# Kernel optimization log

Hardware: AMD Instinct MI355X
Metric: run time of the kernel (lower is better)

## Reference

```python
import jax, jax.numpy as jnp
import numpy as np

B, F, D, K = 16384, 200, 32, 4
H1, H2 = 32, 16
BN_EPS = 1e-3  # keras BatchNormalization default epsilon


def setup_inputs() -> dict:
    key = jax.random.key(0)
    ks = jax.random.split(key, 12)
    inp = {
        "x": jax.random.normal(ks[0], (B, F, D), dtype=jnp.float32),
        "tag_embedding": jax.random.normal(ks[1], (B, D), dtype=jnp.float32),
        "vk_embs": jax.random.normal(ks[2], (D, K), dtype=jnp.float32) * 0.1,
        # tower 1: Dense(D->H1) stacked over K experts, + BN params
        "W1": jax.random.normal(ks[3], (K, D, H1), dtype=jnp.float32) * (1.0 / np.sqrt(D)),
        "b1": jnp.zeros((K, H1), dtype=jnp.float32),
        "g1": jnp.ones((K, H1), dtype=jnp.float32) + 0.1 * jax.random.normal(ks[4], (K, H1), dtype=jnp.float32),
        "be1": 0.1 * jax.random.normal(ks[5], (K, H1), dtype=jnp.float32),
        "m1": 0.1 * jax.random.normal(ks[6], (K, H1), dtype=jnp.float32),
        "v1": jax.random.uniform(ks[7], (K, H1), dtype=jnp.float32, minval=0.5, maxval=1.5),
        # tower 2: Dense(H1->H2) + BN params
        "W2": jax.random.normal(ks[8], (K, H1, H2), dtype=jnp.float32) * (1.0 / np.sqrt(H1)),
        "b2": jnp.zeros((K, H2), dtype=jnp.float32),
        "g2": jnp.ones((K, H2), dtype=jnp.float32) + 0.1 * jax.random.normal(ks[9], (K, H2), dtype=jnp.float32),
        "be2": 0.1 * jax.random.normal(ks[10], (K, H2), dtype=jnp.float32),
        "m2": 0.1 * jax.random.normal(ks[11], (K, H2), dtype=jnp.float32),
        "v2": jnp.ones((K, H2), dtype=jnp.float32),
    }
    return inp


def _bn(h, gamma, beta, mean, var):
    # inference-mode batch norm per expert, broadcast over batch: h [B,K,H]
    return (h - mean) * jax.lax.rsqrt(var + BN_EPS) * gamma + beta


def reference(x, tag_embedding, vk_embs, W1, b1, g1, be1, m1, v1,
              W2, b2, g2, be2, m2, v2):
    scale = 1.0 / jnp.sqrt(jnp.float32(D))
    # attention-pooled per-kernel context (dropout = identity in eval mode)
    vk_scores = jnp.einsum('bfd,dk->bkf', x, vk_embs)          # [B,K,F]
    vk_probs = jax.nn.softmax(vk_scores, axis=-1)
    context = jnp.einsum('bkf,bfd->bkd', vk_probs, x) * scale   # [B,K,D]
    # per-expert MLP towers, batched over K: Dense -> BN -> relu (dropout=id)
    h = jnp.einsum('bkd,kdh->bkh', context, W1) + b1            # [B,K,H1]
    h = jax.nn.relu(_bn(h, g1, be1, m1, v1))
    h = jnp.einsum('bkh,khj->bkj', h, W2) + b2                  # [B,K,H2]
    vk_outs = jax.nn.relu(_bn(h, g2, be2, m2, v2))
    # soft gate from tag embedding
    gate_scores = (tag_embedding @ vk_embs) * scale             # [B,K]
    gate_probs = jax.nn.softmax(gate_scores, axis=-1)[:, :, None]
    user_embedding = jnp.sum(vk_outs * gate_probs, axis=1)      # [B,H2]
    return user_embedding
```

## Files before the change

### kernel.cpp

```cpp
#include <hip/hip_runtime.h>
#include <hip/hip_bf16.h>

#define NF 200
#define ND 32
#define NK 4
#define NH1 32
#define NH2 16
#define BN_EPS 1e-3f

__global__ __launch_bounds__(256) void mvke_fused(
    const float* __restrict__ x, const float* __restrict__ tag,
    const float* __restrict__ vk,
    const float* __restrict__ W1, const float* __restrict__ b1,
    const float* __restrict__ g1, const float* __restrict__ be1,
    const float* __restrict__ m1, const float* __restrict__ v1,
    const float* __restrict__ W2, const float* __restrict__ b2,
    const float* __restrict__ g2, const float* __restrict__ be2,
    const float* __restrict__ m2, const float* __restrict__ v2,
    float* __restrict__ out, int nrows)
{
  __shared__ float w1s[NK*ND*NH1];
  __shared__ float w2s[NK*NH1*NH2];
  __shared__ float a1s[NK*NH1], c1s[NK*NH1];
  __shared__ float a2s[NK*NH2], c2s[NK*NH2];
  __shared__ float ctx_s[4][NK*ND];
  __shared__ float h1_s[4][NK*NH1];

  const int tid = threadIdx.x;
  for (int i = tid; i < NK*ND*NH1; i += 256) w1s[i] = W1[i];
  for (int i = tid; i < NK*NH1*NH2; i += 256) w2s[i] = W2[i];
  if (tid < NK*NH1) {
    const float a = g1[tid] * rsqrtf(v1[tid] + BN_EPS);
    a1s[tid] = a;
    c1s[tid] = (b1[tid] - m1[tid]) * a + be1[tid];
  } else if (tid >= 128 && tid < 128 + NK*NH2) {
    const int t = tid - 128;
    const float a = g2[t] * rsqrtf(v2[t] + BN_EPS);
    a2s[t] = a;
    c2s[t] = (b2[t] - m2[t]) * a + be2[t];
  }

  const int wave = tid >> 6;
  const int lane = tid & 63;
  const int fg   = lane >> 3;
  const int dl   = lane & 7;
  const int row  = blockIdx.x * 4 + wave;
  const bool live = (row < nrows);

  float vkt[NK][4];
  #pragma unroll
  for (int j = 0; j < 4; ++j) {
    const float4 vv = *(const float4*)(vk + (4*dl + j) * NK);
    vkt[0][j] = vv.x; vkt[1][j] = vv.y; vkt[2][j] = vv.z; vkt[3][j] = vv.w;
  }

  const float* xrow = x + (size_t)(live ? row : 0) * (NF*ND);
  const int laneoff = fg*ND + dl*4;

  float cx[NK], cy[NK], cz[NK], cw[NK], ls[NK];
  #pragma unroll
  for (int k = 0; k < NK; ++k) { cx[k]=cy[k]=cz[k]=cw[k]=ls[k]=0.f; }

  for (int it = 0; it < NF/8; ++it) {
    const float4 xa = *(const float4*)(xrow + it*(8*ND) + laneoff);
    #pragma unroll
    for (int k = 0; k < NK; ++k) {
      float t = xa.x*vkt[k][0] + xa.y*vkt[k][1] + xa.z*vkt[k][2] + xa.w*vkt[k][3];
      t += __shfl_xor(t, 1);
      t += __shfl_xor(t, 2);
      t += __shfl_xor(t, 4);
      const float p = __expf(t);
      ls[k] += p;
      cx[k] = fmaf(p, xa.x, cx[k]);
      cy[k] = fmaf(p, xa.y, cy[k]);
      cz[k] = fmaf(p, xa.z, cz[k]);
      cw[k] = fmaf(p, xa.w, cw[k]);
    }
  }

  #pragma unroll
  for (int k = 0; k < NK; ++k) {
    #pragma unroll
    for (int m = 8; m <= 32; m <<= 1) {
      ls[k] += __shfl_xor(ls[k], m);
      cx[k] += __shfl_xor(cx[k], m);
      cy[k] += __shfl_xor(cy[k], m);
      cz[k] += __shfl_xor(cz[k], m);
      cw[k] += __shfl_xor(cw[k], m);
    }
  }

  const float scale = 0.17677669529663687f;
  if (fg == 0) {
    #pragma unroll
    for (int k = 0; k < NK; ++k) {
      const float inv = scale / ls[k];
      float* p = &ctx_s[wave][k*ND + dl*4];
      p[0] = cx[k]*inv; p[1] = cy[k]*inv; p[2] = cz[k]*inv; p[3] = cw[k]*inv;
    }
  }
  __syncthreads();

  #pragma unroll
  for (int rep = 0; rep < 2; ++rep) {
    const int o = lane + rep*64;
    const int k = o >> 5, h = o & 31;
    const float* wp = &w1s[k*(ND*NH1) + h];
    const float* cp = &ctx_s[wave][k*ND];
    float acc = 0.f;
    #pragma unroll
    for (int d = 0; d < ND; ++d) acc = fmaf(cp[d], wp[d*NH1], acc);
    h1_s[wave][o] = fmaxf(fmaf(acc, a1s[o], c1s[o]), 0.f);
  }
  __syncthreads();

  {
    const int k3 = lane >> 4, j3 = lane & 15;
    const float* wp = &w2s[k3*(NH1*NH2) + j3];
    const float* hp = &h1_s[wave][k3*NH1];
    float acc = 0.f;
    #pragma unroll
    for (int h = 0; h < NH1; ++h) acc = fmaf(hp[h], wp[h*NH2], acc);
    const int o = k3*NH2 + j3;
    const float h2v = fmaxf(fmaf(acc, a2s[o], c2s[o]), 0.f);

    const float* tp = tag + (size_t)(live ? row : 0) * ND;
    float gs0=0.f, gs1=0.f, gs2=0.f, gs3=0.f;
    #pragma unroll
    for (int d = 0; d < ND; ++d) {
      const float t = tp[d];
      const float4 vv = *(const float4*)(vk + d*NK);
      gs0 = fmaf(t, vv.x, gs0);
      gs1 = fmaf(t, vv.y, gs1);
      gs2 = fmaf(t, vv.z, gs2);
      gs3 = fmaf(t, vv.w, gs3);
    }
    gs0 *= scale; gs1 *= scale; gs2 *= scale; gs3 *= scale;
    const float mx = fmaxf(fmaxf(gs0, gs1), fmaxf(gs2, gs3));
    const float e0 = __expf(gs0-mx), e1 = __expf(gs1-mx),
                e2 = __expf(gs2-mx), e3 = __expf(gs3-mx);
    const float esum = e0 + e1 + e2 + e3;
    const float ek = (k3 == 0) ? e0 : (k3 == 1) ? e1 : (k3 == 2) ? e2 : e3;

    float val = (ek / esum) * h2v;
    val += __shfl_xor(val, 16);
    val += __shfl_xor(val, 32);
    if (live && lane < NH2) out[(size_t)row*NH2 + lane] = val;
  }
}

extern "C" void kernel_launch(void* const* d_in, const int* in_sizes, int n_in,
                              void* d_out, int out_size, void* d_ws, size_t ws_size,
                              hipStream_t stream) {
  const float* x   = (const float*)d_in[0];
  const float* tag = (const float*)d_in[1];
  const float* vk  = (const float*)d_in[2];
  const float* W1  = (const float*)d_in[3];
  const float* b1  = (const float*)d_in[4];
  const float* g1  = (const float*)d_in[5];
  const float* be1 = (const float*)d_in[6];
  const float* m1  = (const float*)d_in[7];
  const float* v1  = (const float*)d_in[8];
  const float* W2  = (const float*)d_in[9];
  const float* b2  = (const float*)d_in[10];
  const float* g2  = (const float*)d_in[11];
  const float* be2 = (const float*)d_in[12];
  const float* m2  = (const float*)d_in[13];
  const float* v2  = (const float*)d_in[14];
  float* out = (float*)d_out;

  const int nrows = in_sizes[1] / ND;
  const int nblocks = (nrows + 3) / 4;
  mvke_fused<<<nblocks, 256, 0, stream>>>(x, tag, vk, W1, b1, g1, be1, m1, v1,
                                          W2, b2, g2, be2, m2, v2, out, nrows);
}
```

Measured before the change: 124.9 us.

## Split fused kernel into streaming attention-pool and MLP finish kernels via workspace

Splits the fused kernel in two. The first streams x and computes the unnormalized softmax-weighted context and the sums per row, with no shared memory and a 5-deep batch of float4 loads per iteration. The second reads that workspace and runs the BN-MLP towers and the gate. The aim is to lift the streaming kernel's occupancy and memory-level parallelism, since it no longer carries large shared-memory weight tiles or block barriers. The cost is an extra launch plus a workspace round-trip of about 8.6 MB. The fused path is kept as a fallback when the workspace is too small.

```diff
diff --git a/kernel.cpp b/kernel.cpp
--- a/kernel.cpp
+++ b/kernel.cpp
@@ -7,6 +7,181 @@
 #define NH1 32
 #define NH2 16
 #define BN_EPS 1e-3f
+#define WS_PER_ROW 132
+
+__global__ __launch_bounds__(256) void mvke_stream(
+    const float* __restrict__ x, const float* __restrict__ vk,
+    float* __restrict__ ws, int nrows)
+{
+  const int tid  = threadIdx.x;
+  const int wave = tid >> 6;
+  const int lane = tid & 63;
+  const int fg   = lane >> 3;
+  const int dl   = lane & 7;
+  const int row  = blockIdx.x * 4 + wave;
+  if (row >= nrows) return;
+
+  float vkt[NK][4];
+  #pragma unroll
+  for (int j = 0; j < 4; ++j) {
+    const float4 vv = *(const float4*)(vk + (4*dl + j) * NK);
+    vkt[0][j] = vv.x; vkt[1][j] = vv.y; vkt[2][j] = vv.z; vkt[3][j] = vv.w;
+  }
+
+  const float* xrow = x + (size_t)row * (NF*ND);
+  const int laneoff = fg*ND + dl*4;
+
+  float cx[NK], cy[NK], cz[NK], cw[NK], ls[NK];
+  #pragma unroll
+  for (int k = 0; k < NK; ++k) { cx[k]=cy[k]=cz[k]=cw[k]=ls[k]=0.f; }
+
+  for (int it = 0; it < 5; ++it) {
+    float4 xa[5];
+    #pragma unroll
+    for (int j = 0; j < 5; ++j)
+      xa[j] = *(const float4*)(xrow + (it*5 + j)*(8*ND) + laneoff);
+    #pragma unroll
+    for (int j = 0; j < 5; ++j) {
+      #pragma unroll
+      for (int k = 0; k < NK; ++k) {
+        float t = xa[j].x*vkt[k][0] + xa[j].y*vkt[k][1]
+                + xa[j].z*vkt[k][2] + xa[j].w*vkt[k][3];
+        t += __shfl_xor(t, 1);
+        t += __shfl_xor(t, 2);
+        t += __shfl_xor(t, 4);
+        const float p = __expf(t);
+        ls[k] += p;
+        cx[k] = fmaf(p, xa[j].x, cx[k]);
+        cy[k] = fmaf(p, xa[j].y, cy[k]);
+        cz[k] = fmaf(p, xa[j].z, cz[k]);
+        cw[k] = fmaf(p, xa[j].w, cw[k]);
+      }
+    }
+  }
+
+  #pragma unroll
+  for (int k = 0; k < NK; ++k) {
+    #pragma unroll
+    for (int m = 8; m <= 32; m <<= 1) {
+      ls[k] += __shfl_xor(ls[k], m);
+      cx[k] += __shfl_xor(cx[k], m);
+      cy[k] += __shfl_xor(cy[k], m);
+      cz[k] += __shfl_xor(cz[k], m);
+      cw[k] += __shfl_xor(cw[k], m);
+    }
+  }
+
+  float* wr = ws + (size_t)row * WS_PER_ROW;
+  if (fg == 0) {
+    #pragma unroll
+    for (int k = 0; k < NK; ++k) {
+      float4 v; v.x = cx[k]; v.y = cy[k]; v.z = cz[k]; v.w = cw[k];
+      *(float4*)(wr + k*ND + dl*4) = v;
+    }
+    if (dl == 0) {
+      float4 l4; l4.x = ls[0]; l4.y = ls[1]; l4.z = ls[2]; l4.w = ls[3];
+      *(float4*)(wr + NK*ND) = l4;
+    }
+  }
+}
+
+__global__ __launch_bounds__(256) void mvke_finish(
+    const float* __restrict__ ws, const float* __restrict__ tag,
+    const float* __restrict__ vk,
+    const float* __restrict__ W1, const float* __restrict__ b1,
+    const float* __restrict__ g1, const float* __restrict__ be1,
+    const float* __restrict__ m1, const float* __restrict__ v1,
+    const float* __restrict__ W2, const float* __restrict__ b2,
+    const float* __restrict__ g2, const float* __restrict__ be2,
+    const float* __restrict__ m2, const float* __restrict__ v2,
+    float* __restrict__ out, int nrows)
+{
+  __shared__ float w1s[NK*ND*NH1];
+  __shared__ float w2s[NK*NH1*NH2];
+  __shared__ float a1s[NK*NH1], c1s[NK*NH1];
+  __shared__ float a2s[NK*NH2], c2s[NK*NH2];
+  __shared__ float ctx_s[4][NK*ND];
+  __shared__ float h1_s[4][NK*NH1];
+
+  const int tid = threadIdx.x;
+  for (int i = tid; i < NK*ND*NH1; i += 256) w1s[i] = W1[i];
+  for (int i = tid; i < NK*NH1*NH2; i += 256) w2s[i] = W2[i];
+  if (tid < NK*NH1) {
+    const float a = g1[tid] * rsqrtf(v1[tid] + BN_EPS);
+    a1s[tid] = a;
+    c1s[tid] = (b1[tid] - m1[tid]) * a + be1[tid];
+  } else if (tid >= 128 && tid < 128 + NK*NH2) {
+    const int t = tid - 128;
+    const float a = g2[t] * rsqrtf(v2[t] + BN_EPS);
+    a2s[t] = a;
+    c2s[t] = (b2[t] - m2[t]) * a + be2[t];
+  }
+
+  const int wave = tid >> 6;
+  const int lane = tid & 63;
+  const int row  = blockIdx.x * 4 + wave;
+  const bool live = (row < nrows);
+  const float scale = 0.17677669529663687f;
+
+  const float* wr = ws + (size_t)(live ? row : 0) * WS_PER_ROW;
+  {
+    const float  r0 = wr[lane];
+    const float  r1 = wr[64 + lane];
+    const float4 l4 = *(const float4*)(wr + NK*ND);
+    const float inv0 = scale / ((lane      >> 5) == 0 ? l4.x : l4.y);
+    const float inv1 = scale / (((64+lane) >> 5) == 2 ? l4.z : l4.w);
+    ctx_s[wave][lane]      = r0 * inv0;
+    ctx_s[wave][64 + lane] = r1 * inv1;
+  }
+  __syncthreads();
+
+  #pragma unroll
+  for (int rep = 0; rep < 2; ++rep) {
+    const int o = lane + rep*64;
+    const int k = o >> 5, h = o & 31;
+    const float* wp = &w1s[k*(ND*NH1) + h];
+    const float* cp = &ctx_s[wave][k*ND];
+    float acc = 0.f;
+    #pragma unroll
+    for (int d = 0; d < ND; ++d) acc = fmaf(cp[d], wp[d*NH1], acc);
+    h1_s[wave][o] = fmaxf(fmaf(acc, a1s[o], c1s[o]), 0.f);
+  }
+  __syncthreads();
+
+  {
+    const int k3 = lane >> 4, j3 = lane & 15;
+    const float* wp = &w2s[k3*(NH1*NH2) + j3];
+    const float* hp = &h1_s[wave][k3*NH1];
+    float acc = 0.f;
+    #pragma unroll
+    for (int h = 0; h < NH1; ++h) acc = fmaf(hp[h], wp[h*NH2], acc);
+    const int o = k3*NH2 + j3;
+    const float h2v = fmaxf(fmaf(acc, a2s[o], c2s[o]), 0.f);
+
+    const float* tp = tag + (size_t)(live ? row : 0) * ND;
+    float gs0=0.f, gs1=0.f, gs2=0.f, gs3=0.f;
+    #pragma unroll
+    for (int d = 0; d < ND; ++d) {
+      const float t = tp[d];
+      const float4 vv = *(const float4*)(vk + d*NK);
+      gs0 = fmaf(t, vv.x, gs0);
+      gs1 = fmaf(t, vv.y, gs1);
+      gs2 = fmaf(t, vv.z, gs2);
+      gs3 = fmaf(t, vv.w, gs3);
+    }
+    gs0 *= scale; gs1 *= scale; gs2 *= scale; gs3 *= scale;
+    const float mx = fmaxf(fmaxf(gs0, gs1), fmaxf(gs2, gs3));
+    const float e0 = __expf(gs0-mx), e1 = __expf(gs1-mx),
+                e2 = __expf(gs2-mx), e3 = __expf(gs3-mx);
+    const float esum = e0 + e1 + e2 + e3;
+    const float ek = (k3 == 0) ? e0 : (k3 == 1) ? e1 : (k3 == 2) ? e2 : e3;
+
+    float val = (ek / esum) * h2v;
+    val += __shfl_xor(val, 16);
+    val += __shfl_xor(val, 32);
+    if (live && lane < NH2) out[(size_t)row*NH2 + lane] = val;
+  }
+}
 
 __global__ __launch_bounds__(256) void mvke_fused(
     const float* __restrict__ x, const float* __restrict__ tag,
@@ -171,6 +346,15 @@
 
   const int nrows = in_sizes[1] / ND;
   const int nblocks = (nrows + 3) / 4;
-  mvke_fused<<<nblocks, 256, 0, stream>>>(x, tag, vk, W1, b1, g1, be1, m1, v1,
-                                          W2, b2, g2, be2, m2, v2, out, nrows);
+  const size_t ws_need = (size_t)nrows * WS_PER_ROW * sizeof(float);
+
+  if (ws_size >= ws_need) {
+    mvke_stream<<<nblocks, 256, 0, stream>>>(x, vk, (float*)d_ws, nrows);
+    mvke_finish<<<nblocks, 256, 0, stream>>>((const float*)d_ws, tag, vk,
+                                             W1, b1, g1, be1, m1, v1,
+                                             W2, b2, g2, be2, m2, v2, out, nrows);
+  } else {
+    mvke_fused<<<nblocks, 256, 0, stream>>>(x, tag, vk, W1, b1, g1, be1, m1, v1,
+                                            W2, b2, g2, be2, m2, v2, out, nrows);
+  }
 }
```

Result: slower. 143.7 us (+15.1%).
